# Kernel tuning notes

Hardware: AMD Instinct MI355X
Metric: run time of the kernel (lower is better)

Reference implementation:

```python
import jax, jax.numpy as jnp
import numpy as np

B, S, H = 4, 2048, 1024
E = 8
INTER = 2816  # round(4.0*1024*2/3)=2731 -> next multiple of 256


def setup_inputs() -> dict:
    key = jax.random.key(0)
    k1, k2, k3, k4 = jax.random.split(key, 4)
    x = jax.random.normal(k1, (B, S, H), dtype=jnp.float32)
    gate_w = jax.random.normal(k2, (E, H), dtype=jnp.float32) * 0.02
    w_gate_up = jax.random.normal(k3, (E, H, 2 * INTER), dtype=jnp.float32) * 0.02
    w_down = jax.random.normal(k4, (E, INTER, H), dtype=jnp.float32) * 0.02
    return {"x": x, "gate_w": gate_w, "w_gate_up": w_gate_up, "w_down": w_down, "top_k": 2}


def _moe(x, gate_w, w_gate_up, w_down, top_k):
    Bx, Sx, Hx = x.shape
    Ex = gate_w.shape[0]
    T = Bx * Sx
    # Router
    logits = jnp.einsum('bsh,eh->bse', x, gate_w)
    probs = jax.nn.softmax(logits.astype(jnp.float32), axis=-1)  # [B,S,E] fp32
    topk_vals, topk_idx = jax.lax.top_k(probs, top_k)             # [B,S,K]
    topk_w = topk_vals / jnp.clip(topk_vals.sum(-1, keepdims=True), 1e-8)
    importance = probs.mean((0, 1))                               # [E]
    onehot = jax.nn.one_hot(topk_idx, Ex, dtype=probs.dtype)      # [B,S,K,E]
    sel_mask = onehot.sum(-2)                                     # [B,S,E] 0/1 (topk unique)
    load = sel_mask.sum((0, 1)) / (T * top_k)
    aux_loss = (Ex * (importance * load)).sum()
    # Dense combine weights per token/expert (scatter_add equivalent)
    W_full = (onehot * topk_w[..., None]).sum(-2)                 # [B,S,E]
    x_flat = x.reshape(T, Hx)
    W_flat = W_full.reshape(T, Ex).astype(x.dtype)
    out = jnp.zeros_like(x_flat)
    for e in range(Ex):  # fixed small expert loop
        gu = x_flat @ w_gate_up[e]                                # [T, 2I]
        g, u = jnp.split(gu, 2, axis=-1)
        y = (jax.nn.silu(g) * u) @ w_down[e]                      # [T, H]
        out = out + y * W_flat[:, e:e + 1]
    return out.reshape(Bx, Sx, Hx), aux_loss


def reference(x, gate_w, w_gate_up, w_down, top_k):
    return _moe(x, gate_w, w_gate_up, w_down, int(top_k))
```

## Files before the change

### kernel.cpp

```cpp
#include <hip/hip_runtime.h>

#define E_ 8
#define H_ 1024
#define I_ 2816
#define GU_ 5632
#define T_ 8192
#define NBR_ 2048

typedef __attribute__((ext_vector_type(8))) __bf16 bf16x8;
typedef __attribute__((ext_vector_type(4))) float f32x4;
typedef __attribute__((ext_vector_type(8))) unsigned short u16x8;
typedef unsigned short u16;

__device__ __forceinline__ float bf2f(u16 u) {
  union { unsigned int i; float f; } v; v.i = ((unsigned int)u) << 16; return v.f;
}
__device__ __forceinline__ u16 f2bf(float f) {
  union { float f; unsigned int i; } v; v.f = f;
  unsigned int r = v.i + 0x7fffu + ((v.i >> 16) & 1u);
  return (u16)(r >> 16);
}
__device__ __forceinline__ void gld16(const void* g, void* l) {
  __builtin_amdgcn_global_load_lds((const __attribute__((address_space(1))) void*)g,
                                   (__attribute__((address_space(3))) void*)l, 16, 0, 0);
}

__global__ __launch_bounds__(256) void k_router(
    const float* __restrict__ x, const float* __restrict__ gw,
    float* __restrict__ part_imp, int* __restrict__ part_cnt,
    int* __restrict__ tok_e, float* __restrict__ tok_w,
    u16* __restrict__ xb)
{
  __shared__ float s_imp[8];
  __shared__ int s_cnt[8];
  if (threadIdx.x < 8) { s_imp[threadIdx.x] = 0.f; s_cnt[threadIdx.x] = 0; }
  __syncthreads();

  const int t = blockIdx.x * 4 + (threadIdx.x >> 6);
  const int lane = threadIdx.x & 63;
  const float* xr = x + (size_t)t * H_;
  const f32x4* xp = (const f32x4*)(xr + lane * 16);
  f32x4 v0 = xp[0], v1 = xp[1], v2 = xp[2], v3 = xp[3];
  float xv[16];
#pragma unroll
  for (int b = 0; b < 4; ++b) { xv[b] = v0[b]; xv[4+b] = v1[b]; xv[8+b] = v2[b]; xv[12+b] = v3[b]; }
  u16x8 o0, o1;
#pragma unroll
  for (int j = 0; j < 8; ++j) { o0[j] = f2bf(xv[j]); o1[j] = f2bf(xv[8 + j]); }
  *(u16x8*)(xb + (size_t)t * H_ + lane * 16) = o0;
  *(u16x8*)(xb + (size_t)t * H_ + lane * 16 + 8) = o1;

  float lg[8];
#pragma unroll
  for (int e = 0; e < 8; ++e) {
    const f32x4* gp = (const f32x4*)(gw + e * H_ + lane * 16);
    float s = 0.f;
#pragma unroll
    for (int a = 0; a < 4; ++a) {
      f32x4 g4 = gp[a];
#pragma unroll
      for (int b = 0; b < 4; ++b) s += xv[a * 4 + b] * g4[b];
    }
    lg[e] = s;
  }
#pragma unroll
  for (int e = 0; e < 8; ++e)
#pragma unroll
    for (int off = 32; off; off >>= 1) lg[e] += __shfl_xor(lg[e], off);

  float m = lg[0];
#pragma unroll
  for (int e = 1; e < 8; ++e) m = fmaxf(m, lg[e]);
  float p[8], sum = 0.f;
#pragma unroll
  for (int e = 0; e < 8; ++e) { p[e] = __expf(lg[e] - m); sum += p[e]; }
  float inv = 1.f / sum;
#pragma unroll
  for (int e = 0; e < 8; ++e) p[e] *= inv;
  int e0 = 0;
#pragma unroll
  for (int e = 1; e < 8; ++e) if (p[e] > p[e0]) e0 = e;
  int e1 = (e0 == 0) ? 1 : 0;
#pragma unroll
  for (int e = 0; e < 8; ++e) if (e != e0 && p[e] > p[e1]) e1 = e;
  float d = 1.f / (p[e0] + p[e1]);
  if (lane == 0) {
#pragma unroll
    for (int e = 0; e < 8; ++e) atomicAdd(&s_imp[e], p[e]);
    atomicAdd(&s_cnt[e0], 1);
    atomicAdd(&s_cnt[e1], 1);
    tok_e[2 * t] = e0; tok_e[2 * t + 1] = e1;
    tok_w[2 * t] = p[e0] * d; tok_w[2 * t + 1] = p[e1] * d;
  }
  __syncthreads();
  if (threadIdx.x < 8) {
    part_imp[blockIdx.x * 8 + threadIdx.x] = s_imp[threadIdx.x];
    part_cnt[blockIdx.x * 8 + threadIdx.x] = s_cnt[threadIdx.x];
  }
}

__global__ __launch_bounds__(512) void k_reduce_scan(
    const float* __restrict__ part_imp, const int* __restrict__ part_cnt,
    int* __restrict__ counts, int* __restrict__ offsets, float* __restrict__ out)
{
  const int w = threadIdx.x >> 6, lane = threadIdx.x & 63;
  float si = 0.f; int sc = 0;
  for (int b = lane; b < NBR_; b += 64) { si += part_imp[b * 8 + w]; sc += part_cnt[b * 8 + w]; }
#pragma unroll
  for (int off = 32; off; off >>= 1) { si += __shfl_xor(si, off); sc += __shfl_xor(sc, off); }
  __shared__ float fimp[8];
  __shared__ int fcnt[8];
  if (lane == 0) { fimp[w] = si; fcnt[w] = sc; }
  __syncthreads();
  if (threadIdx.x == 0) {
    int off = 0; float aux = 0.f;
#pragma unroll
    for (int e = 0; e < 8; ++e) {
      counts[e] = fcnt[e]; offsets[e] = off; off += fcnt[e];
      aux += fimp[e] * (float)fcnt[e];
    }
    out[(size_t)T_ * H_] = 8.f * aux / ((float)T_ * (float)(2 * T_));
  }
}

__global__ __launch_bounds__(256) void k_scatter(
    const int* __restrict__ tok_e, const float* __restrict__ tok_w,
    const int* __restrict__ offsets, int* __restrict__ cursors,
    int* __restrict__ rows, float* __restrict__ wslot, int* __restrict__ t2s)
{
  __shared__ int lcnt[8], lbase[8];
  if (threadIdx.x < 8) lcnt[threadIdx.x] = 0;
  __syncthreads();
  const int t = blockIdx.x * 256 + threadIdx.x;
  const int e0 = tok_e[2 * t], e1 = tok_e[2 * t + 1];
  const int p0 = atomicAdd(&lcnt[e0], 1);
  const int p1 = atomicAdd(&lcnt[e1], 1);
  __syncthreads();
  if (threadIdx.x < 8) lbase[threadIdx.x] = atomicAdd(&cursors[threadIdx.x], lcnt[threadIdx.x]);
  __syncthreads();
  const int s0 = offsets[e0] + lbase[e0] + p0;
  const int s1 = offsets[e1] + lbase[e1] + p1;
  rows[s0] = t; wslot[s0] = tok_w[2 * t];     t2s[2 * t] = s0;
  rows[s1] = t; wslot[s1] = tok_w[2 * t + 1]; t2s[2 * t + 1] = s1;
}

__global__ __launch_bounds__(256) void k_transpose(
    const float* __restrict__ src, u16* __restrict__ dst, int R, int C)
{
  __shared__ float tile[32][33];
  const int z = blockIdx.z;
  const int c0 = blockIdx.x * 32, r0 = blockIdx.y * 32;
  const float* s = src + (size_t)z * R * C;
  u16* d = dst + (size_t)z * R * C;
  const int tx = threadIdx.x & 31, ty = threadIdx.x >> 5;
#pragma unroll
  for (int i = 0; i < 4; ++i)
    tile[ty + i * 8][tx] = s[(size_t)(r0 + ty + i * 8) * C + c0 + tx];
  __syncthreads();
#pragma unroll
  for (int i = 0; i < 4; ++i)
    d[(size_t)(c0 + ty + i * 8) * R + r0 + tx] = f2bf(tile[tx][ty + i * 8]);
}

__global__ __launch_bounds__(512, 2) void k_gemm1(
    const u16* __restrict__ xb, const u16* __restrict__ wgu_t,
    const int* __restrict__ counts, const int* __restrict__ offsets,
    const int* __restrict__ rows, const float* __restrict__ wslot,
    u16* __restrict__ act)
{
  extern __shared__ char sh[];
  const int bid = blockIdx.x;
  const int l = (bid & 7) * 704 + (bid >> 3);
  const int e = l / 704;
  const int rm = l - e * 704;
  const int yb = rm >> 5, xx = rm & 31;
  const int cnt = counts[e];
  const int m0 = xx * 256;
  if (m0 >= cnt) return;
  const int seg = offsets[e];
  const int segLast = seg + cnt - 1;
  const int n0 = yb * 128;

  const int tid = threadIdx.x;
  const int wid = tid >> 6, lane = tid & 63;
  const int srow = tid >> 3;
  const int scol = (((tid & 7) ^ (srow & 7)) * 8);

  const u16* wge = wgu_t + (size_t)e * GU_ * H_;

  const u16* aPtr[4];
#pragma unroll
  for (int i = 0; i < 4; ++i) {
    int slot = seg + m0 + i * 64 + srow;
    aPtr[i] = xb + (size_t)rows[slot > segLast ? segLast : slot] * H_ + scol;
  }
  const u16* bPtr[4];
#pragma unroll
  for (int i = 0; i < 4; ++i) {
    int r = i * 64 + srow;
    int gr = (r < 128) ? (n0 + r) : (I_ + n0 + (r - 128));
    bPtr[i] = wge + (size_t)gr * H_ + scol;
  }

  const int wm = (wid >> 2) * 128;
  const int wn = (wid & 3) * 32;

  f32x4 accg[8][2], accu[8][2];
#pragma unroll
  for (int i = 0; i < 8; ++i)
#pragma unroll
    for (int j = 0; j < 2; ++j) { accg[i][j] = (f32x4){0.f,0.f,0.f,0.f}; accu[i][j] = (f32x4){0.f,0.f,0.f,0.f}; }

#define STAGE_A1(b, kt) { const int k0 = (kt) * 64;                               \
    char* dst = sh + (b) * 65536 + tid * 16;                                      \
    _Pragma("unroll") for (int i = 0; i < 4; ++i) gld16(aPtr[i] + k0, dst + i * 8192); }
#define STAGE_B1(b, kt) { const int k0 = (kt) * 64;                               \
    char* dst = sh + (b) * 65536 + 32768 + tid * 16;                              \
    _Pragma("unroll") for (int i = 0; i < 4; ++i) gld16(bPtr[i] + k0, dst + i * 8192); }

  const int NT = H_ / 64;
  STAGE_A1(0, 0); STAGE_B1(0, 0); STAGE_A1(1, 1);
  asm volatile("s_waitcnt vmcnt(4)" ::: "memory");
  __builtin_amdgcn_s_barrier();

  int cur = 0;
#pragma unroll 2
  for (int t = 0; t < NT; ++t) {
    STAGE_B1(cur ^ 1, (t + 1 < NT) ? t + 1 : NT - 1);
    const u16* As = (const u16*)(sh + cur * 65536);
    const u16* Bs = As + 16384;
#pragma unroll
    for (int ks = 0; ks < 2; ++ks) {
      const int koff = (ks * 32 + (lane >> 4) * 8) ^ ((lane & 7) * 8);
      bf16x8 a[8], bg[2], bu[2];
#pragma unroll
      for (int mf = 0; mf < 8; ++mf)
        a[mf] = *(const bf16x8*)(As + (wm + mf * 16 + (lane & 15)) * 64 + koff);
#pragma unroll
      for (int nf = 0; nf < 2; ++nf) {
        bg[nf] = *(const bf16x8*)(Bs + (wn + nf * 16 + (lane & 15)) * 64 + koff);
        bu[nf] = *(const bf16x8*)(Bs + (128 + wn + nf * 16 + (lane & 15)) * 64 + koff);
      }
      __builtin_amdgcn_s_setprio(1);
#pragma unroll
      for (int mf = 0; mf < 8; ++mf)
#pragma unroll
        for (int nf = 0; nf < 2; ++nf) {
          accg[mf][nf] = __builtin_amdgcn_mfma_f32_16x16x32_bf16(a[mf], bg[nf], accg[mf][nf], 0, 0, 0);
          accu[mf][nf] = __builtin_amdgcn_mfma_f32_16x16x32_bf16(a[mf], bu[nf], accu[mf][nf], 0, 0, 0);
        }
      __builtin_amdgcn_s_setprio(0);
    }
    asm volatile("" ::: "memory");
    __builtin_amdgcn_s_barrier();
    STAGE_A1(cur, (t + 2 < NT) ? t + 2 : NT - 1);
    asm volatile("s_waitcnt vmcnt(4)" ::: "memory");
    __builtin_amdgcn_s_barrier();
    cur ^= 1;
  }
  asm volatile("s_waitcnt vmcnt(0)" ::: "memory");
#undef STAGE_A1
#undef STAGE_B1

#pragma unroll
  for (int mf = 0; mf < 8; ++mf)
#pragma unroll
    for (int reg = 0; reg < 4; ++reg) {
      const int r = wm + mf * 16 + (lane >> 4) * 4 + reg;
      if (m0 + r >= cnt) continue;
      const int slot = seg + m0 + r;
      const float w = wslot[slot];
#pragma unroll
      for (int nf = 0; nf < 2; ++nf) {
        float g = accg[mf][nf][reg];
        float u = accu[mf][nf][reg];
        float sv = (g / (1.f + __expf(-g))) * u * w;
        act[(size_t)slot * I_ + n0 + wn + nf * 16 + (lane & 15)] = f2bf(sv);
      }
    }
}

__global__ __launch_bounds__(512, 2) void k_gemm2(
    const u16* __restrict__ act, const u16* __restrict__ wd_t,
    const int* __restrict__ counts, const int* __restrict__ offsets,
    u16* __restrict__ y)
{
  extern __shared__ char sh[];
  const int bid = blockIdx.x;
  const int l = (bid & 7) * 128 + (bid >> 3);
  const int e = l >> 7;
  const int rm = l & 127;
  const int yb = rm >> 5, xx = rm & 31;
  const int cnt = counts[e];
  const int m0 = xx * 256;
  if (m0 >= cnt) return;
  const int seg = offsets[e];
  const int segLast = seg + cnt - 1;
  const int n0 = yb * 256;

  const int tid = threadIdx.x;
  const int wid = tid >> 6, lane = tid & 63;
  const int srow = tid >> 3;
  const int scol = (((tid & 7) ^ (srow & 7)) * 8);

  const u16* wde = wd_t + (size_t)e * H_ * I_;

  const u16* aPtr[4];
#pragma unroll
  for (int i = 0; i < 4; ++i) {
    int slot = seg + m0 + i * 64 + srow;
    aPtr[i] = act + (size_t)(slot > segLast ? segLast : slot) * I_ + scol;
  }
  const u16* bPtr[4];
#pragma unroll
  for (int i = 0; i < 4; ++i)
    bPtr[i] = wde + (size_t)(n0 + i * 64 + srow) * I_ + scol;

  const int wm = (wid >> 2) * 128;
  const int wn = (wid & 3) * 64;

  f32x4 acc[8][4];
#pragma unroll
  for (int i = 0; i < 8; ++i)
#pragma unroll
    for (int j = 0; j < 4; ++j) acc[i][j] = (f32x4){0.f,0.f,0.f,0.f};

#define STAGE_A2(b, kt) { const int k0 = (kt) * 64;                               \
    char* dst = sh + (b) * 65536 + tid * 16;                                      \
    _Pragma("unroll") for (int i = 0; i < 4; ++i) gld16(aPtr[i] + k0, dst + i * 8192); }
#define STAGE_B2(b, kt) { const int k0 = (kt) * 64;                               \
    char* dst = sh + (b) * 65536 + 32768 + tid * 16;                              \
    _Pragma("unroll") for (int i = 0; i < 4; ++i) gld16(bPtr[i] + k0, dst + i * 8192); }

  const int NT = I_ / 64;
  STAGE_A2(0, 0); STAGE_B2(0, 0); STAGE_A2(1, 1);
  asm volatile("s_waitcnt vmcnt(4)" ::: "memory");
  __builtin_amdgcn_s_barrier();

  int cur = 0;
#pragma unroll 2
  for (int t = 0; t < NT; ++t) {
    STAGE_B2(cur ^ 1, (t + 1 < NT) ? t + 1 : NT - 1);
    const u16* As = (const u16*)(sh + cur * 65536);
    const u16* Bs = As + 16384;
#pragma unroll
    for (int ks = 0; ks < 2; ++ks) {
      const int koff = (ks * 32 + (lane >> 4) * 8) ^ ((lane & 7) * 8);
      bf16x8 a[8], b[4];
#pragma unroll
      for (int mf = 0; mf < 8; ++mf)
        a[mf] = *(const bf16x8*)(As + (wm + mf * 16 + (lane & 15)) * 64 + koff);
#pragma unroll
      for (int nf = 0; nf < 4; ++nf)
        b[nf] = *(const bf16x8*)(Bs + (wn + nf * 16 + (lane & 15)) * 64 + koff);
      __builtin_amdgcn_s_setprio(1);
#pragma unroll
      for (int mf = 0; mf < 8; ++mf)
#pragma unroll
        for (int nf = 0; nf < 4; ++nf)
          acc[mf][nf] = __builtin_amdgcn_mfma_f32_16x16x32_bf16(a[mf], b[nf], acc[mf][nf], 0, 0, 0);
      __builtin_amdgcn_s_setprio(0);
    }
    asm volatile("" ::: "memory");
    __builtin_amdgcn_s_barrier();
    STAGE_A2(cur, (t + 2 < NT) ? t + 2 : NT - 1);
    asm volatile("s_waitcnt vmcnt(4)" ::: "memory");
    __builtin_amdgcn_s_barrier();
    cur ^= 1;
  }
  asm volatile("s_waitcnt vmcnt(0)" ::: "memory");
#undef STAGE_A2
#undef STAGE_B2

#pragma unroll
  for (int mf = 0; mf < 8; ++mf)
#pragma unroll
    for (int reg = 0; reg < 4; ++reg) {
      const int r = wm + mf * 16 + (lane >> 4) * 4 + reg;
      if (m0 + r >= cnt) continue;
      const int slot = seg + m0 + r;
#pragma unroll
      for (int nf = 0; nf < 4; ++nf)
        y[(size_t)slot * H_ + n0 + wn + nf * 16 + (lane & 15)] = f2bf(acc[mf][nf][reg]);
    }
}

__global__ __launch_bounds__(256) void k_combine(
    const u16* __restrict__ y, const int* __restrict__ t2s, float* __restrict__ out)
{
  const size_t idx = ((size_t)blockIdx.x * 256 + threadIdx.x) * 8;
  const int t = (int)(idx >> 10);
  const int h = (int)(idx & 1023);
  const int s0 = t2s[2 * t], s1 = t2s[2 * t + 1];
  u16x8 a = *(const u16x8*)(y + (size_t)s0 * H_ + h);
  u16x8 b = *(const u16x8*)(y + (size_t)s1 * H_ + h);
  f32x4 o0, o1;
#pragma unroll
  for (int j = 0; j < 4; ++j) o0[j] = bf2f(a[j]) + bf2f(b[j]);
#pragma unroll
  for (int j = 0; j < 4; ++j) o1[j] = bf2f(a[4 + j]) + bf2f(b[4 + j]);
  *(f32x4*)(out + idx) = o0;
  *(f32x4*)(out + idx + 4) = o1;
}

extern "C" void kernel_launch(void* const* d_in, const int* in_sizes, int n_in,
                              void* d_out, int out_size, void* d_ws, size_t ws_size,
                              hipStream_t stream)
{
  const float* x   = (const float*)d_in[0];
  const float* gw  = (const float*)d_in[1];
  const float* wgu = (const float*)d_in[2];
  const float* wd  = (const float*)d_in[3];
  float* out = (float*)d_out;
  char* ws = (char*)d_ws;

  const size_t off_wgu_t = 0;
  const size_t off_wd_t  = off_wgu_t + (size_t)E_ * GU_ * H_ * 2;
  const size_t off_xb    = off_wd_t  + (size_t)E_ * H_ * I_ * 2;
  const size_t off_act   = off_xb    + (size_t)T_ * H_ * 2;
  const size_t off_ctrl  = off_act   + (size_t)2 * T_ * I_ * 2;
  const size_t need = off_ctrl + 128 + 5 * 65536;
  if (ws_size < need) return;

  u16* wgu_t = (u16*)(ws + off_wgu_t);
  u16* wd_t  = (u16*)(ws + off_wd_t);
  u16* xb    = (u16*)(ws + off_xb);
  u16* act   = (u16*)(ws + off_act);
  u16* y     = (u16*)(ws + off_wgu_t);
  float* part_imp = (float*)(ws + off_act);
  int*   part_cnt = (int*)(ws + off_act + (size_t)NBR_ * 8 * 4);
  char* ctrl = ws + off_ctrl;
  int*   counts  = (int*)(ctrl + 0);
  int*   cursors = (int*)(ctrl + 32);
  int*   offsets = (int*)(ctrl + 64);
  int*   tok_e   = (int*)(ctrl + 128);
  float* tok_w   = (float*)(ctrl + 128 + 1 * 65536);
  int*   rows    = (int*)(ctrl + 128 + 2 * 65536);
  float* wslot   = (float*)(ctrl + 128 + 3 * 65536);
  int*   t2s     = (int*)(ctrl + 128 + 4 * 65536);

  static bool attr_done = false;
  if (!attr_done) {
    hipFuncSetAttribute((const void*)k_gemm1, hipFuncAttributeMaxDynamicSharedMemorySize, 131072);
    hipFuncSetAttribute((const void*)k_gemm2, hipFuncAttributeMaxDynamicSharedMemorySize, 131072);
    attr_done = true;
  }

  hipMemsetAsync(ctrl, 0, 96, stream);
  hipLaunchKernelGGL(k_transpose, dim3(GU_ / 32, H_ / 32, E_), dim3(256), 0, stream, wgu, wgu_t, H_, GU_);
  hipLaunchKernelGGL(k_transpose, dim3(H_ / 32, I_ / 32, E_), dim3(256), 0, stream, wd, wd_t, I_, H_);
  hipLaunchKernelGGL(k_router, dim3(NBR_), dim3(256), 0, stream, x, gw, part_imp, part_cnt, tok_e, tok_w, xb);
  hipLaunchKernelGGL(k_reduce_scan, dim3(1), dim3(512), 0, stream, part_imp, part_cnt, counts, offsets, out);
  hipLaunchKernelGGL(k_scatter, dim3(T_ / 256), dim3(256), 0, stream, tok_e, tok_w, offsets, cursors, rows, wslot, t2s);
  hipLaunchKernelGGL(k_gemm1, dim3(32 * (I_ / 128) * E_), dim3(512), 131072, stream, xb, wgu_t, counts, offsets, rows, wslot, act);
  hipLaunchKernelGGL(k_gemm2, dim3(32 * (H_ / 256) * E_), dim3(512), 131072, stream, act, wd_t, counts, offsets, y);
  hipLaunchKernelGGL(k_combine, dim3((T_ * H_) / (256 * 8)), dim3(256), 0, stream, y, t2s, out);
}
```

Baseline: 546.5 us.

## Restructure MoE GEMM main loops into 4-phase ping-pong schedule with interleaved loads

Both grouped GEMM kernels now split each K-tile into four MFMA phases over half-tiles of A and B. The global-to-LDS loads for the next tile are spread between those phases, separated by barriers and sched_barriers. The aim is to hide memory latency behind matrix math, in the style of a ping-pong / 8-wave schedule, instead of issuing all loads in bulk. The cost is more barriers per iteration, and correctness of the buffer reuse depends on careful wait counts.

```diff
diff --git a/kernel.cpp b/kernel.cpp
--- a/kernel.cpp
+++ b/kernel.cpp
@@ -24,6 +24,11 @@
   __builtin_amdgcn_global_load_lds((const __attribute__((address_space(1))) void*)g,
                                    (__attribute__((address_space(3))) void*)l, 16, 0, 0);
 }
+
+#define BAR() __builtin_amdgcn_s_barrier()
+#define SB0() __builtin_amdgcn_sched_barrier(0)
+#define LGKM0() asm volatile("s_waitcnt lgkmcnt(0)" ::: "memory")
+#define VMC(n) asm volatile("s_waitcnt vmcnt(" #n ")" ::: "memory")
 
 __global__ __launch_bounds__(256) void k_router(
     const float* __restrict__ x, const float* __restrict__ gw,
@@ -182,7 +187,7 @@
   const int n0 = yb * 128;
 
   const int tid = threadIdx.x;
-  const int wid = tid >> 6, lane = tid & 63;
+  const int wid = tid >> 6, lane = tid & 63, l15 = lane & 15;
   const int srow = tid >> 3;
   const int scol = (((tid & 7) ^ (srow & 7)) * 8);
 
@@ -211,56 +216,99 @@
 #pragma unroll
     for (int j = 0; j < 2; ++j) { accg[i][j] = (f32x4){0.f,0.f,0.f,0.f}; accu[i][j] = (f32x4){0.f,0.f,0.f,0.f}; }
 
-#define STAGE_A1(b, kt) { const int k0 = (kt) * 64;                               \
-    char* dst = sh + (b) * 65536 + tid * 16;                                      \
-    _Pragma("unroll") for (int i = 0; i < 4; ++i) gld16(aPtr[i] + k0, dst + i * 8192); }
-#define STAGE_B1(b, kt) { const int k0 = (kt) * 64;                               \
-    char* dst = sh + (b) * 65536 + 32768 + tid * 16;                              \
-    _Pragma("unroll") for (int i = 0; i < 4; ++i) gld16(bPtr[i] + k0, dst + i * 8192); }
+#define G1_BG(b, kt) { const int k0 = (kt) * 64; char* d = sh + (b) * 65536 + 32768 + tid * 16; \
+    gld16(bPtr[0] + k0, d); gld16(bPtr[1] + k0, d + 8192); }
+#define G1_BU(b, kt) { const int k0 = (kt) * 64; char* d = sh + (b) * 65536 + 49152 + tid * 16; \
+    gld16(bPtr[2] + k0, d); gld16(bPtr[3] + k0, d + 8192); }
+#define G1_A(b, kt)  { const int k0 = (kt) * 64; char* d = sh + (b) * 65536 + tid * 16;        \
+    gld16(aPtr[0] + k0, d); gld16(aPtr[1] + k0, d + 8192);                                     \
+    gld16(aPtr[2] + k0, d + 16384); gld16(aPtr[3] + k0, d + 24576); }
 
   const int NT = H_ / 64;
-  STAGE_A1(0, 0); STAGE_B1(0, 0); STAGE_A1(1, 1);
-  asm volatile("s_waitcnt vmcnt(4)" ::: "memory");
-  __builtin_amdgcn_s_barrier();
+  G1_BG(0, 0) G1_BU(0, 0) G1_A(0, 0)
+  G1_BG(1, 1) G1_BU(1, 1) G1_A(1, 1)
+  VMC(8);
+  BAR(); SB0();
 
   int cur = 0;
-#pragma unroll 2
   for (int t = 0; t < NT; ++t) {
-    STAGE_B1(cur ^ 1, (t + 1 < NT) ? t + 1 : NT - 1);
+    const int nx = (t + 2 < NT) ? t + 2 : NT - 1;
     const u16* As = (const u16*)(sh + cur * 65536);
     const u16* Bs = As + 16384;
+    bf16x8 af[2][4], bg[2][2], bu[2][2];
 #pragma unroll
     for (int ks = 0; ks < 2; ++ks) {
       const int koff = (ks * 32 + (lane >> 4) * 8) ^ ((lane & 7) * 8);
-      bf16x8 a[8], bg[2], bu[2];
-#pragma unroll
-      for (int mf = 0; mf < 8; ++mf)
-        a[mf] = *(const bf16x8*)(As + (wm + mf * 16 + (lane & 15)) * 64 + koff);
+#pragma unroll
+      for (int mf = 0; mf < 4; ++mf)
+        af[ks][mf] = *(const bf16x8*)(As + (wm + mf * 16 + l15) * 64 + koff);
 #pragma unroll
       for (int nf = 0; nf < 2; ++nf) {
-        bg[nf] = *(const bf16x8*)(Bs + (wn + nf * 16 + (lane & 15)) * 64 + koff);
-        bu[nf] = *(const bf16x8*)(Bs + (128 + wn + nf * 16 + (lane & 15)) * 64 + koff);
+        bg[ks][nf] = *(const bf16x8*)(Bs + (wn + nf * 16 + l15) * 64 + koff);
+        bu[ks][nf] = *(const bf16x8*)(Bs + (128 + wn + nf * 16 + l15) * 64 + koff);
       }
-      __builtin_amdgcn_s_setprio(1);
-#pragma unroll
-      for (int mf = 0; mf < 8; ++mf)
-#pragma unroll
-        for (int nf = 0; nf < 2; ++nf) {
-          accg[mf][nf] = __builtin_amdgcn_mfma_f32_16x16x32_bf16(a[mf], bg[nf], accg[mf][nf], 0, 0, 0);
-          accu[mf][nf] = __builtin_amdgcn_mfma_f32_16x16x32_bf16(a[mf], bu[nf], accu[mf][nf], 0, 0, 0);
-        }
-      __builtin_amdgcn_s_setprio(0);
-    }
-    asm volatile("" ::: "memory");
-    __builtin_amdgcn_s_barrier();
-    STAGE_A1(cur, (t + 2 < NT) ? t + 2 : NT - 1);
-    asm volatile("s_waitcnt vmcnt(4)" ::: "memory");
-    __builtin_amdgcn_s_barrier();
+    }
+    BAR(); SB0(); LGKM0(); SB0();
+    __builtin_amdgcn_s_setprio(1);
+#pragma unroll
+    for (int ks = 0; ks < 2; ++ks)
+#pragma unroll
+      for (int mf = 0; mf < 4; ++mf)
+#pragma unroll
+        for (int nf = 0; nf < 2; ++nf)
+          accg[mf][nf] = __builtin_amdgcn_mfma_f32_16x16x32_bf16(af[ks][mf], bg[ks][nf], accg[mf][nf], 0, 0, 0);
+    __builtin_amdgcn_s_setprio(0);
+    BAR(); SB0();
+    G1_BG(cur, nx)
+    BAR(); SB0();
+    __builtin_amdgcn_s_setprio(1);
+#pragma unroll
+    for (int ks = 0; ks < 2; ++ks)
+#pragma unroll
+      for (int mf = 0; mf < 4; ++mf)
+#pragma unroll
+        for (int nf = 0; nf < 2; ++nf)
+          accu[mf][nf] = __builtin_amdgcn_mfma_f32_16x16x32_bf16(af[ks][mf], bu[ks][nf], accu[mf][nf], 0, 0, 0);
+    __builtin_amdgcn_s_setprio(0);
+    BAR(); SB0();
+#pragma unroll
+    for (int ks = 0; ks < 2; ++ks) {
+      const int koff = (ks * 32 + (lane >> 4) * 8) ^ ((lane & 7) * 8);
+#pragma unroll
+      for (int mf = 0; mf < 4; ++mf)
+        af[ks][mf] = *(const bf16x8*)(As + (wm + 64 + mf * 16 + l15) * 64 + koff);
+    }
+    G1_BU(cur, nx)
+    BAR(); SB0(); LGKM0(); SB0();
+    __builtin_amdgcn_s_setprio(1);
+#pragma unroll
+    for (int ks = 0; ks < 2; ++ks)
+#pragma unroll
+      for (int mf = 0; mf < 4; ++mf)
+#pragma unroll
+        for (int nf = 0; nf < 2; ++nf)
+          accg[4 + mf][nf] = __builtin_amdgcn_mfma_f32_16x16x32_bf16(af[ks][mf], bg[ks][nf], accg[4 + mf][nf], 0, 0, 0);
+    __builtin_amdgcn_s_setprio(0);
+    BAR(); SB0();
+    G1_A(cur, nx)
+    BAR(); SB0();
+    __builtin_amdgcn_s_setprio(1);
+#pragma unroll
+    for (int ks = 0; ks < 2; ++ks)
+#pragma unroll
+      for (int mf = 0; mf < 4; ++mf)
+#pragma unroll
+        for (int nf = 0; nf < 2; ++nf)
+          accu[4 + mf][nf] = __builtin_amdgcn_mfma_f32_16x16x32_bf16(af[ks][mf], bu[ks][nf], accu[4 + mf][nf], 0, 0, 0);
+    __builtin_amdgcn_s_setprio(0);
+    BAR(); SB0();
+    VMC(8); SB0();
     cur ^= 1;
   }
-  asm volatile("s_waitcnt vmcnt(0)" ::: "memory");
-#undef STAGE_A1
-#undef STAGE_B1
+  VMC(0);
+#undef G1_BG
+#undef G1_BU
+#undef G1_A
 
 #pragma unroll
   for (int mf = 0; mf < 8; ++mf)
@@ -275,7 +323,7 @@
         float g = accg[mf][nf][reg];
         float u = accu[mf][nf][reg];
         float sv = (g / (1.f + __expf(-g))) * u * w;
-        act[(size_t)slot * I_ + n0 + wn + nf * 16 + (lane & 15)] = f2bf(sv);
+        act[(size_t)slot * I_ + n0 + wn + nf * 16 + l15] = f2bf(sv);
       }
     }
 }
@@ -299,7 +347,7 @@
   const int n0 = yb * 256;
 
   const int tid = threadIdx.x;
-  const int wid = tid >> 6, lane = tid & 63;
+  const int wid = tid >> 6, lane = tid & 63, l15 = lane & 15;
   const int srow = tid >> 3;
   const int scol = (((tid & 7) ^ (srow & 7)) * 8);
 
@@ -325,52 +373,97 @@
 #pragma unroll
     for (int j = 0; j < 4; ++j) acc[i][j] = (f32x4){0.f,0.f,0.f,0.f};
 
-#define STAGE_A2(b, kt) { const int k0 = (kt) * 64;                               \
-    char* dst = sh + (b) * 65536 + tid * 16;                                      \
-    _Pragma("unroll") for (int i = 0; i < 4; ++i) gld16(aPtr[i] + k0, dst + i * 8192); }
-#define STAGE_B2(b, kt) { const int k0 = (kt) * 64;                               \
-    char* dst = sh + (b) * 65536 + 32768 + tid * 16;                              \
-    _Pragma("unroll") for (int i = 0; i < 4; ++i) gld16(bPtr[i] + k0, dst + i * 8192); }
+#define G2_BL(b, kt) { const int k0 = (kt) * 64; char* d = sh + (b) * 65536 + 32768 + tid * 16; \
+    gld16(bPtr[0] + k0, d); gld16(bPtr[1] + k0, d + 8192); }
+#define G2_BH(b, kt) { const int k0 = (kt) * 64; char* d = sh + (b) * 65536 + 49152 + tid * 16; \
+    gld16(bPtr[2] + k0, d); gld16(bPtr[3] + k0, d + 8192); }
+#define G2_A(b, kt)  { const int k0 = (kt) * 64; char* d = sh + (b) * 65536 + tid * 16;        \
+    gld16(aPtr[0] + k0, d); gld16(aPtr[1] + k0, d + 8192);                                     \
+    gld16(aPtr[2] + k0, d + 16384); gld16(aPtr[3] + k0, d + 24576); }
 
   const int NT = I_ / 64;
-  STAGE_A2(0, 0); STAGE_B2(0, 0); STAGE_A2(1, 1);
-  asm volatile("s_waitcnt vmcnt(4)" ::: "memory");
-  __builtin_amdgcn_s_barrier();
+  G2_BL(0, 0) G2_BH(0, 0) G2_A(0, 0)
+  G2_BL(1, 1) G2_BH(1, 1) G2_A(1, 1)
+  VMC(8);
+  BAR(); SB0();
 
   int cur = 0;
-#pragma unroll 2
   for (int t = 0; t < NT; ++t) {
-    STAGE_B2(cur ^ 1, (t + 1 < NT) ? t + 1 : NT - 1);
+    const int nx = (t + 2 < NT) ? t + 2 : NT - 1;
     const u16* As = (const u16*)(sh + cur * 65536);
     const u16* Bs = As + 16384;
+    bf16x8 af[2][4], b[2][4];
 #pragma unroll
     for (int ks = 0; ks < 2; ++ks) {
       const int koff = (ks * 32 + (lane >> 4) * 8) ^ ((lane & 7) * 8);
-      bf16x8 a[8], b[4];
-#pragma unroll
-      for (int mf = 0; mf < 8; ++mf)
-        a[mf] = *(const bf16x8*)(As + (wm + mf * 16 + (lane & 15)) * 64 + koff);
+#pragma unroll
+      for (int mf = 0; mf < 4; ++mf)
+        af[ks][mf] = *(const bf16x8*)(As + (wm + mf * 16 + l15) * 64 + koff);
 #pragma unroll
       for (int nf = 0; nf < 4; ++nf)
-        b[nf] = *(const bf16x8*)(Bs + (wn + nf * 16 + (lane & 15)) * 64 + koff);
-      __builtin_amdgcn_s_setprio(1);
-#pragma unroll
-      for (int mf = 0; mf < 8; ++mf)
-#pragma unroll
-        for (int nf = 0; nf < 4; ++nf)
-          acc[mf][nf] = __builtin_amdgcn_mfma_f32_16x16x32_bf16(a[mf], b[nf], acc[mf][nf], 0, 0, 0);
-      __builtin_amdgcn_s_setprio(0);
-    }
-    asm volatile("" ::: "memory");
-    __builtin_amdgcn_s_barrier();
-    STAGE_A2(cur, (t + 2 < NT) ? t + 2 : NT - 1);
-    asm volatile("s_waitcnt vmcnt(4)" ::: "memory");
-    __builtin_amdgcn_s_barrier();
+        b[ks][nf] = *(const bf16x8*)(Bs + (wn + nf * 16 + l15) * 64 + koff);
+    }
+    BAR(); SB0(); LGKM0(); SB0();
+    __builtin_amdgcn_s_setprio(1);
+#pragma unroll
+    for (int ks = 0; ks < 2; ++ks)
+#pragma unroll
+      for (int mf = 0; mf < 4; ++mf)
+#pragma unroll
+        for (int nf = 0; nf < 2; ++nf)
+          acc[mf][nf] = __builtin_amdgcn_mfma_f32_16x16x32_bf16(af[ks][mf], b[ks][nf], acc[mf][nf], 0, 0, 0);
+    __builtin_amdgcn_s_setprio(0);
+    BAR(); SB0();
+    G2_BL(cur, nx)
+    BAR(); SB0();
+    __builtin_amdgcn_s_setprio(1);
+#pragma unroll
+    for (int ks = 0; ks < 2; ++ks)
+#pragma unroll
+      for (int mf = 0; mf < 4; ++mf)
+#pragma unroll
+        for (int nf = 2; nf < 4; ++nf)
+          acc[mf][nf] = __builtin_amdgcn_mfma_f32_16x16x32_bf16(af[ks][mf], b[ks][nf], acc[mf][nf], 0, 0, 0);
+    __builtin_amdgcn_s_setprio(0);
+    BAR(); SB0();
+#pragma unroll
+    for (int ks = 0; ks < 2; ++ks) {
+      const int koff = (ks * 32 + (lane >> 4) * 8) ^ ((lane & 7) * 8);
+#pragma unroll
+      for (int mf = 0; mf < 4; ++mf)
+        af[ks][mf] = *(const bf16x8*)(As + (wm + 64 + mf * 16 + l15) * 64 + koff);
+    }
+    G2_BH(cur, nx)
+    BAR(); SB0(); LGKM0(); SB0();
+    __builtin_amdgcn_s_setprio(1);
+#pragma unroll
+    for (int ks = 0; ks < 2; ++ks)
+#pragma unroll
+      for (int mf = 0; mf < 4; ++mf)
+#pragma unroll
+        for (int nf = 0; nf < 2; ++nf)
+          acc[4 + mf][nf] = __builtin_amdgcn_mfma_f32_16x16x32_bf16(af[ks][mf], b[ks][nf], acc[4 + mf][nf], 0, 0, 0);
+    __builtin_amdgcn_s_setprio(0);
+    BAR(); SB0();
+    G2_A(cur, nx)
+    BAR(); SB0();
+    __builtin_amdgcn_s_setprio(1);
+#pragma unroll
+    for (int ks = 0; ks < 2; ++ks)
+#pragma unroll
+      for (int mf = 0; mf < 4; ++mf)
+#pragma unroll
+        for (int nf = 2; nf < 4; ++nf)
+          acc[4 + mf][nf] = __builtin_amdgcn_mfma_f32_16x16x32_bf16(af[ks][mf], b[ks][nf], acc[4 + mf][nf], 0, 0, 0);
+    __builtin_amdgcn_s_setprio(0);
+    BAR(); SB0();
+    VMC(8); SB0();
     cur ^= 1;
   }
-  asm volatile("s_waitcnt vmcnt(0)" ::: "memory");
-#undef STAGE_A2
-#undef STAGE_B2
+  VMC(0);
+#undef G2_BL
+#undef G2_BH
+#undef G2_A
 
 #pragma unroll
   for (int mf = 0; mf < 8; ++mf)
@@ -381,7 +474,7 @@
       const int slot = seg + m0 + r;
 #pragma unroll
       for (int nf = 0; nf < 4; ++nf)
-        y[(size_t)slot * H_ + n0 + wn + nf * 16 + (lane & 15)] = f2bf(acc[mf][nf][reg]);
+        y[(size_t)slot * H_ + n0 + wn + nf * 16 + l15] = f2bf(acc[mf][nf][reg]);
     }
 }
 
```

New measurement: 594.2 us. 8.7% more time.
